# Kernel tuning notes

Hardware: AMD Instinct MI355X
Metric: run time of the kernel (lower is better)

The kernel has to match this reference:

```python
import jax, jax.numpy as jnp
import numpy as np

N_NODES = 100000


def _gcn_conv(x, W, b, src, dst, n_nodes):
    # PyG GCNConv: linear transform, add self-loops, symmetric deg normalization,
    # scatter-add aggregation at target nodes, then bias.
    h = x @ W  # [N, out]
    loops = jnp.arange(n_nodes, dtype=src.dtype)
    src2 = jnp.concatenate([src, loops])
    dst2 = jnp.concatenate([dst, loops])
    ones = jnp.ones(src2.shape[0], dtype=h.dtype)
    deg = jax.ops.segment_sum(ones, dst2, num_segments=n_nodes)  # in-degree incl. self-loop
    dinv = jnp.where(deg > 0, jax.lax.rsqrt(deg), 0.0)
    norm = dinv[src2] * dinv[dst2]  # [E+N]
    msg = h[src2] * norm[:, None]  # gather + weight, [E+N, out]
    out = jax.ops.segment_sum(msg, dst2, num_segments=n_nodes)
    return out + b


def setup_inputs() -> dict:
    key = jax.random.key(0)
    k1, k2, k3, k4 = jax.random.split(key, 4)
    n, e, f, h, c = N_NODES, 3200000, 512, 16, 32
    x = jax.random.normal(k1, (n, f), dtype=jnp.float32)
    edge_index = jax.random.randint(k2, (2, e), 0, n, dtype=jnp.int64)
    W1 = jax.random.normal(k3, (f, h), dtype=jnp.float32) * (1.0 / np.sqrt(f))
    b1 = jnp.zeros((h,), dtype=jnp.float32)
    W2 = jax.random.normal(k4, (h, c), dtype=jnp.float32) * (1.0 / np.sqrt(h))
    b2 = jnp.zeros((c,), dtype=jnp.float32)
    return {"x": x, "edge_index": edge_index, "W1": W1, "b1": b1, "W2": W2, "b2": b2}


def reference(x, edge_index, W1, b1, W2, b2):
    src, dst = edge_index[0], edge_index[1]
    n = x.shape[0]
    h = _gcn_conv(x, W1, b1, src, dst, n)
    h = jax.nn.relu(h)
    h = _gcn_conv(h, W2, b2, src, dst, n)
    return jax.nn.log_softmax(h, axis=1)
```

## Files before the change

kernel.cpp:

```cpp
#include <hip/hip_runtime.h>
#include <hip/hip_bf16.h>


#define BK 128
#define BKSH 7
#define MAXNB 1024
#define CHUNK 12800
#define SLAB 5120

typedef __attribute__((ext_vector_type(8))) short bf16x8;
typedef __attribute__((ext_vector_type(4))) float f32x4;

union ABpack { bf16x8 v; int i[4]; };

__device__ __forceinline__ int cvt2(float a, float b) {
    __hip_bfloat162 h = __float22bfloat162_rn(make_float2(a, b));
    return *reinterpret_cast<int*>(&h);
}
__device__ __forceinline__ unsigned short cvt1(float a) {
    __hip_bfloat16 h = __float2bfloat16(a);
    return *reinterpret_cast<unsigned short*>(&h);
}
__device__ __forceinline__ float b2f(unsigned short s) {
    return __uint_as_float(((unsigned)s) << 16);
}

__device__ __forceinline__ void load_lds16(const float* g, void* l) {
    __builtin_amdgcn_global_load_lds((const __attribute__((address_space(1))) void*)g,
                                     (__attribute__((address_space(3))) void*)l, 16, 0, 0);
}

__global__ __launch_bounds__(256) void k_init_cur(int* __restrict__ gcur, int NB) {
    int i = blockIdx.x * 256 + threadIdx.x;
    if (i < NB) gcur[i] = i * SLAB;
}

__global__ __launch_bounds__(256) void k_fill2(const int* __restrict__ src,
                                               const int* __restrict__ dst,
                                               int* __restrict__ gcur,
                                               int* __restrict__ gq, int E, int NB) {
    __shared__ int h[MAXNB];
    __shared__ int base[MAXNB];
    for (int t = threadIdx.x; t < NB; t += 256) h[t] = 0;
    __syncthreads();
    int e0 = blockIdx.x * CHUNK, e1 = min(E, e0 + CHUNK);
    for (int e = e0 + threadIdx.x; e < e1; e += 256)
        atomicAdd(&h[dst[e] >> BKSH], 1);
    __syncthreads();
    for (int t = threadIdx.x; t < NB; t += 256) {
        int c = h[t];
        base[t] = c ? atomicAdd(&gcur[t], c) : 0;
    }
    __syncthreads();
    for (int t = threadIdx.x; t < NB; t += 256) h[t] = 0;
    __syncthreads();
    for (int e = e0 + threadIdx.x; e < e1; e += 256) {
        int d = dst[e], b = d >> BKSH;
        int loc = atomicAdd(&h[b], 1);
        gq[base[b] + loc] = (src[e] << BKSH) | (d & (BK - 1));
    }
}

__global__ __launch_bounds__(256) void k_sortb(const int* __restrict__ gq,
                                               const int* __restrict__ gcur,
                                               int* __restrict__ gq2,
                                               int* __restrict__ offs,
                                               int* __restrict__ nend,
                                               float* __restrict__ dinv, int n) {
    __shared__ int cnt[BK];
    __shared__ int cur[BK];
    int b = blockIdx.x;
    int p0 = b * SLAB, p1 = gcur[b];
    if (threadIdx.x < BK) cnt[threadIdx.x] = 0;
    __syncthreads();
    for (int p = p0 + threadIdx.x; p < p1; p += 256)
        atomicAdd(&cnt[__builtin_nontemporal_load(gq + p) & (BK - 1)], 1);
    __syncthreads();
    if (threadIdx.x < BK) cur[threadIdx.x] = cnt[threadIdx.x];
    __syncthreads();
    for (int o = 1; o < BK; o <<= 1) {
        int v = (threadIdx.x < BK && threadIdx.x >= o) ? cur[threadIdx.x - o] : 0;
        __syncthreads();
        if (threadIdx.x < BK) cur[threadIdx.x] += v;
        __syncthreads();
    }
    if (threadIdx.x < BK) {
        int c = cnt[threadIdx.x];
        int excl = cur[threadIdx.x] - c;
        int node = (b << BKSH) + threadIdx.x;
        if (node < n) {
            offs[node] = p0 + excl;
            nend[node] = p0 + excl + c;
            dinv[node] = rsqrtf((float)(c + 1));
        }
        cur[threadIdx.x] = excl;
    }
    __syncthreads();
    for (int p = p0 + threadIdx.x; p < p1; p += 256) {
        int e = __builtin_nontemporal_load(gq + p);
        int loc = atomicAdd(&cur[e & (BK - 1)], 1);
        gq2[p0 + loc] = e >> BKSH;
    }
}

__global__ __launch_bounds__(256) void k_gemm_mfma(const float* __restrict__ x,
                                                   const float* __restrict__ W1,
                                                   const float* __restrict__ dinv,
                                                   unsigned short* __restrict__ gs1,
                                                   int n) {
    const int lane = threadIdx.x & 63;
    const int r = lane & 15;
    const int g4 = lane >> 4;
    const int wid = blockIdx.x * 4 + (threadIdx.x >> 6);
    const int nw = gridDim.x * 4;

    ABpack wf[16];
#pragma unroll
    for (int s = 0; s < 16; ++s) {
        int kb = s * 32 + g4 * 8;
#pragma unroll
        for (int j = 0; j < 4; ++j)
            wf[s].i[j] = cvt2(W1[(size_t)(kb + 2 * j) * 16 + r],
                              W1[(size_t)(kb + 2 * j + 1) * 16 + r]);
    }

    const int ntiles = (n + 15) >> 4;
    for (int tile = wid; tile < ntiles; tile += nw) {
        int m0 = tile << 4;
        int arow = m0 + r;
        if (arow >= n) arow = n - 1;
        const float* xp = x + (size_t)arow * 512 + g4 * 8;
        f32x4 acc = {0.f, 0.f, 0.f, 0.f};
#pragma unroll
        for (int s = 0; s < 16; ++s) {
            f32x4 f0 = __builtin_nontemporal_load(reinterpret_cast<const f32x4*>(xp + s * 32));
            f32x4 f1 = __builtin_nontemporal_load(reinterpret_cast<const f32x4*>(xp + s * 32 + 4));
            ABpack ah;
            ah.i[0] = cvt2(f0[0], f0[1]);
            ah.i[1] = cvt2(f0[2], f0[3]);
            ah.i[2] = cvt2(f1[0], f1[1]);
            ah.i[3] = cvt2(f1[2], f1[3]);
            acc = __builtin_amdgcn_mfma_f32_16x16x32_bf16(ah.v, wf[s].v, acc, 0, 0, 0);
        }
#pragma unroll
        for (int j = 0; j < 4; ++j) {
            int crow = m0 + g4 * 4 + j;
            if (crow < n) {
                float dvv = dinv[crow];
                gs1[(size_t)crow * 16 + r] = cvt1(acc[j] * dvv);
            }
        }
    }
}

__global__ __launch_bounds__(256) void k_agg_b(const unsigned short* __restrict__ featb,
                                               const int* __restrict__ gq2,
                                               const int* __restrict__ offs,
                                               const int* __restrict__ nend,
                                               const float* __restrict__ dinv,
                                               const float* __restrict__ bias,
                                               unsigned short* __restrict__ out_b,
                                               int n) {
    int t = blockIdx.x * 256 + threadIdx.x;
    int i = t >> 4, k = t & 15;
    if (i >= n) return;
    float acc = b2f(featb[(size_t)i * 16 + k]);
    int p = offs[i], p1 = nend[i];
    for (; p + 8 <= p1; p += 8) {
        int s0 = __builtin_nontemporal_load(gq2 + p);
        int s1 = __builtin_nontemporal_load(gq2 + p + 1);
        int s2 = __builtin_nontemporal_load(gq2 + p + 2);
        int s3 = __builtin_nontemporal_load(gq2 + p + 3);
        int s4 = __builtin_nontemporal_load(gq2 + p + 4);
        int s5 = __builtin_nontemporal_load(gq2 + p + 5);
        int s6 = __builtin_nontemporal_load(gq2 + p + 6);
        int s7 = __builtin_nontemporal_load(gq2 + p + 7);
        float v0 = b2f(featb[(size_t)s0 * 16 + k]);
        float v1 = b2f(featb[(size_t)s1 * 16 + k]);
        float v2 = b2f(featb[(size_t)s2 * 16 + k]);
        float v3 = b2f(featb[(size_t)s3 * 16 + k]);
        float v4 = b2f(featb[(size_t)s4 * 16 + k]);
        float v5 = b2f(featb[(size_t)s5 * 16 + k]);
        float v6 = b2f(featb[(size_t)s6 * 16 + k]);
        float v7 = b2f(featb[(size_t)s7 * 16 + k]);
        acc += ((v0 + v1) + (v2 + v3)) + ((v4 + v5) + (v6 + v7));
    }
    for (; p < p1; ++p)
        acc += b2f(featb[(size_t)__builtin_nontemporal_load(gq2 + p) * 16 + k]);
    float dvi = dinv[i];
    float v = fmaxf(dvi * acc + bias[k], 0.f) * dvi;
    out_b[(size_t)i * 16 + k] = cvt1(v);
}

__global__ __launch_bounds__(256) void k_agg_out(const unsigned short* __restrict__ featb,
                                                 const int* __restrict__ gq2,
                                                 const int* __restrict__ offs,
                                                 const int* __restrict__ nend,
                                                 const float* __restrict__ dinv,
                                                 const float* __restrict__ W2,
                                                 const float* __restrict__ b2,
                                                 float* __restrict__ out, int n) {
    __shared__ float Ws[16 * 33];
    __shared__ float bs[32];
    __shared__ float As[16][17];
    for (int t = threadIdx.x; t < 512; t += 256) Ws[(t >> 5) * 33 + (t & 31)] = W2[t];
    if (threadIdx.x < 32) bs[threadIdx.x] = b2[threadIdx.x];

    int t = blockIdx.x * 256 + threadIdx.x;
    int i = t >> 4, k = t & 15, nl = threadIdx.x >> 4;
    float acc = 0.f;
    if (i < n) {
        acc = b2f(featb[(size_t)i * 16 + k]);
        int p = offs[i], p1 = nend[i];
        for (; p + 8 <= p1; p += 8) {
            int s0 = __builtin_nontemporal_load(gq2 + p);
            int s1 = __builtin_nontemporal_load(gq2 + p + 1);
            int s2 = __builtin_nontemporal_load(gq2 + p + 2);
            int s3 = __builtin_nontemporal_load(gq2 + p + 3);
            int s4 = __builtin_nontemporal_load(gq2 + p + 4);
            int s5 = __builtin_nontemporal_load(gq2 + p + 5);
            int s6 = __builtin_nontemporal_load(gq2 + p + 6);
            int s7 = __builtin_nontemporal_load(gq2 + p + 7);
            float v0 = b2f(featb[(size_t)s0 * 16 + k]);
            float v1 = b2f(featb[(size_t)s1 * 16 + k]);
            float v2 = b2f(featb[(size_t)s2 * 16 + k]);
            float v3 = b2f(featb[(size_t)s3 * 16 + k]);
            float v4 = b2f(featb[(size_t)s4 * 16 + k]);
            float v5 = b2f(featb[(size_t)s5 * 16 + k]);
            float v6 = b2f(featb[(size_t)s6 * 16 + k]);
            float v7 = b2f(featb[(size_t)s7 * 16 + k]);
            acc += ((v0 + v1) + (v2 + v3)) + ((v4 + v5) + (v6 + v7));
        }
        for (; p < p1; ++p)
            acc += b2f(featb[(size_t)__builtin_nontemporal_load(gq2 + p) * 16 + k]);
        acc *= dinv[i];
    }
    As[nl][k] = acc;
    __syncthreads();
    if (i < n) {
        float v0 = bs[k], v1 = bs[k + 16];
#pragma unroll
        for (int kk = 0; kk < 16; ++kk) {
            float a = As[nl][kk];
            v0 += a * Ws[kk * 33 + k];
            v1 += a * Ws[kk * 33 + k + 16];
        }
        float m = fmaxf(v0, v1);
#pragma unroll
        for (int o = 8; o > 0; o >>= 1) m = fmaxf(m, __shfl_xor(m, o, 16));
        float pp = expf(v0 - m) + expf(v1 - m);
#pragma unroll
        for (int o = 8; o > 0; o >>= 1) pp += __shfl_xor(pp, o, 16);
        float lg = logf(pp);
        float* op = out + (size_t)i * 32;
        op[k] = v0 - m - lg;
        op[k + 16] = v1 - m - lg;
    }
}

__global__ __launch_bounds__(256) void k_zero_i(int* __restrict__ p, int n) {
    int i = blockIdx.x * 256 + threadIdx.x;
    if (i < n) p[i] = 0;
}

__global__ __launch_bounds__(256) void k_count(const int* __restrict__ dst,
                                               int* __restrict__ cnt, int E) {
    int e = blockIdx.x * 256 + threadIdx.x;
    if (e < E) atomicAdd(&cnt[dst[e]], 1);
}

__global__ __launch_bounds__(256) void k_dinv(const int* __restrict__ cnt,
                                              float* __restrict__ dinv, int n) {
    int i = blockIdx.x * 256 + threadIdx.x;
    if (i < n) dinv[i] = rsqrtf((float)(cnt[i] + 1));
}

__global__ __launch_bounds__(256) void k_gemm1(const float* __restrict__ x,
                                               const float* __restrict__ W1,
                                               const float* __restrict__ dinv,
                                               float* __restrict__ h1,
                                               float* __restrict__ r1self, int n) {
    __shared__ float Ws[8192];
    __shared__ float4 Xs[4][512];
    for (int t = threadIdx.x; t < 8192; t += 256) {
        int sa = t ^ (((t >> 9) & 1) << 4);
        Ws[sa] = W1[t];
    }
    __syncthreads();
    const int wave = threadIdx.x >> 6;
    const int lane = threadIdx.x & 63;
    const int q = lane & 15, g = lane >> 4;
    const int sr = lane >> 3, su = lane & 7;
    const int first = blockIdx.x * 4 + wave;
    const int stride = gridDim.x * 4;
    const int ngroups = (n + 7) >> 3;
    if (first >= ngroups) return;
    const int mygroups = (ngroups - first + stride - 1) / stride;
    const int T = mygroups * 4;
    char* xbase = (char*)(&Xs[wave][0]);
    auto stage = [&](int i) {
        int k = i >> 2, c = i & 3;
        int r0 = (first + k * stride) << 3;
        int row = r0 + sr;
        if (row >= n) row = n - 1;
        const float* gp = x + (size_t)row * 512 + c * 128 + su * 4;
        char* lb = xbase + (i & 1) * 4096;
#pragma unroll
        for (int m = 0; m < 4; ++m) load_lds16(gp + m * 32, lb + m * 1024);
    };
    stage(0);
    if (T > 1) stage(1);
    int issued = (T > 1) ? 2 : 1;
    float acc[8];
    const float4* xw = &Xs[wave][0];
    const int flip = (g & 1) << 4;
    for (int i = 0; i < T; ++i) {
        if (i < T - 1) asm volatile("s_waitcnt vmcnt(4)" ::: "memory");
        else           asm volatile("s_waitcnt vmcnt(0)" ::: "memory");
        int c = i & 3;
        const float4* xb = xw + (i & 1) * 256;
        if (c == 0) {
#pragma unroll
            for (int r = 0; r < 8; ++r) acc[r] = 0.f;
        }
        const int aW = 2048 * c + 512 * g + q;
#pragma unroll
        for (int t = 0; t < 8; ++t) {
            int tg = (t + g) & 7;
            float4 xv[8];
#pragma unroll
            for (int r = 0; r < 8; ++r) xv[r] = xb[g * 64 + r * 8 + tg];
            int a0 = aW + 64 * tg;
            float w0 = Ws[(a0) ^ flip];
            float w1 = Ws[(a0 + 16) ^ flip];
            float w2 = Ws[(a0 + 32) ^ flip];
            float w3 = Ws[(a0 + 48) ^ flip];
#pragma unroll
            for (int r = 0; r < 8; ++r)
                acc[r] += xv[r].x * w0 + xv[r].y * w1 + xv[r].z * w2 + xv[r].w * w3;
        }
        if (issued < T) { stage(issued); ++issued; }
        if (c == 3) {
            int r0 = (first + (i >> 2) * stride) << 3;
#pragma unroll
            for (int r = 0; r < 8; ++r) {
                acc[r] += __shfl_xor(acc[r], 16);
                acc[r] += __shfl_xor(acc[r], 32);
            }
            float v0 = 0.f, v1 = 0.f;
#pragma unroll
            for (int r = 0; r < 4; ++r)
                if (g == r) { v0 = acc[r]; v1 = acc[r + 4]; }
            int row0 = r0 + g, row1 = r0 + 4 + g;
            if (row0 < n) {
                h1[(size_t)row0 * 16 + q] = v0;
                if (r1self) { float dv = dinv[row0]; r1self[(size_t)row0 * 16 + q] = v0 * dv * dv; }
            }
            if (row1 < n) {
                h1[(size_t)row1 * 16 + q] = v1;
                if (r1self) { float dv = dinv[row1]; r1self[(size_t)row1 * 16 + q] = v1 * dv * dv; }
            }
        }
    }
}

__global__ __launch_bounds__(256) void k_scatter16(const int* __restrict__ src,
                                                   const int* __restrict__ dst,
                                                   const float* __restrict__ feat,
                                                   const float* __restrict__ dinv,
                                                   float* __restrict__ outf, int total) {
    int t = blockIdx.x * 256 + threadIdx.x;
    if (t >= total) return;
    int e = t >> 4, k = t & 15;
    int s = src[e], d = dst[e];
    float w = dinv[s] * dinv[d];
    unsafeAtomicAdd(&outf[(size_t)d * 16 + k], feat[(size_t)s * 16 + k] * w);
}

__global__ __launch_bounds__(256) void k_relu16(float* __restrict__ r1,
                                                const float* __restrict__ b1, int total) {
    int t = blockIdx.x * 256 + threadIdx.x;
    if (t < total) r1[t] = fmaxf(r1[t] + b1[t & 15], 0.f);
}

__global__ __launch_bounds__(256) void k_self16(const float* __restrict__ feat,
                                                const float* __restrict__ dinv,
                                                float* __restrict__ outf, int total) {
    int t = blockIdx.x * 256 + threadIdx.x;
    if (t >= total) return;
    float dv = dinv[t >> 4];
    outf[t] = feat[t] * dv * dv;
}

__global__ __launch_bounds__(256) void k_out(const float* __restrict__ a,
                                             const float* __restrict__ W2,
                                             const float* __restrict__ b2,
                                             float* __restrict__ out, int n) {
    __shared__ float Ws[16 * 33];
    __shared__ float bs[32];
    for (int t = threadIdx.x; t < 512; t += 256) Ws[(t >> 5) * 33 + (t & 31)] = W2[t];
    if (threadIdx.x < 32) bs[threadIdx.x] = b2[threadIdx.x];
    __syncthreads();
    int t = blockIdx.x * 256 + threadIdx.x;
    int i = t >> 5, c = t & 31;
    if (i >= n) return;
    const float4* ar = reinterpret_cast<const float4*>(a + (size_t)i * 16);
    float acc = bs[c];
#pragma unroll
    for (int kk = 0; kk < 4; ++kk) {
        float4 v = ar[kk];
        acc += v.x * Ws[(4 * kk + 0) * 33 + c];
        acc += v.y * Ws[(4 * kk + 1) * 33 + c];
        acc += v.z * Ws[(4 * kk + 2) * 33 + c];
        acc += v.w * Ws[(4 * kk + 3) * 33 + c];
    }
    float m = acc;
#pragma unroll
    for (int o = 16; o > 0; o >>= 1) m = fmaxf(m, __shfl_xor(m, o, 32));
    float p = expf(acc - m);
#pragma unroll
    for (int o = 16; o > 0; o >>= 1) p += __shfl_xor(p, o, 32);
    out[t] = acc - m - logf(p);
}

extern "C" void kernel_launch(void* const* d_in, const int* in_sizes, int n_in,
                              void* d_out, int out_size, void* d_ws, size_t ws_size,
                              hipStream_t stream) {
    const float* x  = (const float*)d_in[0];
    const int* ei   = (const int*)d_in[1];
    const float* W1 = (const float*)d_in[2];
    const float* b1 = (const float*)d_in[3];
    const float* W2 = (const float*)d_in[4];
    const float* b2 = (const float*)d_in[5];
    float* out = (float*)d_out;

    const int n = in_sizes[0] / 512;
    const int E = in_sizes[1] / 2;
    const int* src = ei;
    const int* dst = ei + E;
    const int NB = (n + BK - 1) >> BKSH;
    const int gfill = (E + CHUNK - 1) / CHUNK;
    const int ntiles = (n + 15) >> 4;
    const int ggemm = (ntiles + 3) / 4;

    float* ws = (float*)d_ws;

    size_t u_dinv  = 0;
    size_t u_foffs = u_dinv + n;
    size_t u_nend  = u_foffs + n;
    size_t u_gcur  = u_nend + n;
    size_t u_gq    = u_gcur + NB;
    size_t u_gq2   = u_gq + (size_t)NB * SLAB;
    size_t u_h1    = u_gq2 + (size_t)NB * SLAB;
    size_t u_r1    = u_h1 + 16 * (size_t)n;
    size_t need    = (u_r1 + 16 * (size_t)n) * 4;

    if (ws_size >= need && NB <= MAXNB) {
        float* dinv = ws + u_dinv;
        int* offs   = (int*)(ws + u_foffs);
        int* nend   = (int*)(ws + u_nend);
        int* gcur   = (int*)(ws + u_gcur);
        int* gq     = (int*)(ws + u_gq);
        int* gq2    = (int*)(ws + u_gq2);
        unsigned short* gs1b = (unsigned short*)(ws + u_h1);
        unsigned short* r1sb = (unsigned short*)(ws + u_r1);

        k_init_cur<<<(NB + 255) / 256, 256, 0, stream>>>(gcur, NB);
        k_fill2   <<<gfill, 256, 0, stream>>>(src, dst, gcur, gq, E, NB);
        k_sortb   <<<NB, 256, 0, stream>>>(gq, gcur, gq2, offs, nend, dinv, n);
        k_gemm_mfma<<<ggemm, 256, 0, stream>>>(x, W1, dinv, gs1b, n);
        k_agg_b   <<<(n * 16 + 255) / 256, 256, 0, stream>>>(gs1b, gq2, offs, nend,
                                                             dinv, b1, r1sb, n);
        k_agg_out <<<(n * 16 + 255) / 256, 256, 0, stream>>>(r1sb, gq2, offs, nend,
                                                             dinv, W2, b2, out, n);
    } else {
        float* dinv = ws;
        float* h1   = ws + n;
        float* r1   = ws + n + 16 * (size_t)n;
        int* cnt    = (int*)h1;
        float* agg2r = h1;

        const int total1 = E * 16;
        k_zero_i   <<<(n + 255) / 256, 256, 0, stream>>>(cnt, n);
        k_count    <<<(E + 255) / 256, 256, 0, stream>>>(dst, cnt, E);
        k_dinv     <<<(n + 255) / 256, 256, 0, stream>>>(cnt, dinv, n);
        k_gemm1    <<<1024, 256, 0, stream>>>(x, W1, dinv, h1, r1, n);
        k_scatter16<<<(total1 + 255) / 256, 256, 0, stream>>>(src, dst, h1, dinv, r1, total1);
        k_relu16   <<<(n * 16 + 255) / 256, 256, 0, stream>>>(r1, b1, n * 16);
        k_self16   <<<(n * 16 + 255) / 256, 256, 0, stream>>>(r1, dinv, agg2r, n * 16);
        k_scatter16<<<(total1 + 255) / 256, 256, 0, stream>>>(src, dst, r1, dinv, agg2r, total1);
        k_out      <<<(n * 32 + 255) / 256, 256, 0, stream>>>(agg2r, W2, b2, out, n);
    }
}
```

Before: 240.4 us.

## Stage X tiles through double-buffered swizzled LDS with split-K across waves in GEMM

The first-layer GEMM now streams each 16-row tile of x into a double-buffered LDS buffer with direct-to-LDS loads and an XOR swizzle. The four waves each take a quarter of K and combine partial sums through shared memory. The grid is fixed at 512 blocks with a prefetch of the next tile, meant to overlap HBM reads with compute and cut per-wave register use for W. The fill chunk size also shrinks, giving more fill blocks. In exchange it adds barriers, a reduction step and a separate tail path for row counts that are not a multiple of 16.

Result: slower. 249.2 us (+3.7%).

```diff
diff --git a/kernel.cpp b/kernel.cpp
--- a/kernel.cpp
+++ b/kernel.cpp
@@ -5,7 +5,7 @@
 #define BK 128
 #define BKSH 7
 #define MAXNB 1024
-#define CHUNK 12800
+#define CHUNK 3200
 #define SLAB 5120
 
 typedef __attribute__((ext_vector_type(8))) short bf16x8;
@@ -108,39 +108,107 @@
                                                    const float* __restrict__ dinv,
                                                    unsigned short* __restrict__ gs1,
                                                    int n) {
-    const int lane = threadIdx.x & 63;
+    __shared__ char Xs[2][32768];
+    __shared__ f32x4 red[256];
+    const int tid = threadIdx.x;
+    const int w = tid >> 6;
+    const int lane = tid & 63;
     const int r = lane & 15;
     const int g4 = lane >> 4;
-    const int wid = blockIdx.x * 4 + (threadIdx.x >> 6);
-    const int nw = gridDim.x * 4;
-
-    ABpack wf[16];
-#pragma unroll
-    for (int s = 0; s < 16; ++s) {
-        int kb = s * 32 + g4 * 8;
+
+    ABpack wf[4];
+#pragma unroll
+    for (int sl = 0; sl < 4; ++sl) {
+        int kb = (w * 4 + sl) * 32 + g4 * 8;
 #pragma unroll
         for (int j = 0; j < 4; ++j)
-            wf[s].i[j] = cvt2(W1[(size_t)(kb + 2 * j) * 16 + r],
-                              W1[(size_t)(kb + 2 * j + 1) * 16 + r]);
-    }
-
-    const int ntiles = (n + 15) >> 4;
-    for (int tile = wid; tile < ntiles; tile += nw) {
-        int m0 = tile << 4;
-        int arow = m0 + r;
-        if (arow >= n) arow = n - 1;
-        const float* xp = x + (size_t)arow * 512 + g4 * 8;
+            wf[sl].i[j] = cvt2(W1[(size_t)(kb + 2 * j) * 16 + r],
+                               W1[(size_t)(kb + 2 * j + 1) * 16 + r]);
+    }
+    asm volatile("s_waitcnt vmcnt(0)" ::: "memory");
+
+    auto stage = [&](int tile, int buf) {
+        const char* gp = (const char*)x + (size_t)tile * 32768;
+        char* lb = &Xs[buf][0];
+#pragma unroll
+        for (int c = 0; c < 8; ++c) {
+            int o = c * 4096 + tid * 16;
+            int g = o ^ (((o >> 11) & 7) << 4);
+            load_lds16((const float*)(gp + g), lb + o);
+        }
+    };
+
+    const int ntf = n >> 4;
+    int tile = blockIdx.x;
+    const int stride = gridDim.x;
+    if (tile < ntf) stage(tile, 0);
+    int buf = 0;
+    const int swz = (r & 7) << 4;
+
+    for (; tile < ntf; tile += stride) {
+        int nxt = tile + stride;
+        if (nxt < ntf) {
+            stage(nxt, buf ^ 1);
+            asm volatile("s_waitcnt vmcnt(8)" ::: "memory");
+        } else {
+            asm volatile("s_waitcnt vmcnt(0)" ::: "memory");
+        }
+        __builtin_amdgcn_s_barrier();
+        const char* lb = &Xs[buf][0];
         f32x4 acc = {0.f, 0.f, 0.f, 0.f};
 #pragma unroll
-        for (int s = 0; s < 16; ++s) {
-            f32x4 f0 = __builtin_nontemporal_load(reinterpret_cast<const f32x4*>(xp + s * 32));
-            f32x4 f1 = __builtin_nontemporal_load(reinterpret_cast<const f32x4*>(xp + s * 32 + 4));
+        for (int sl = 0; sl < 4; ++sl) {
+            int byte0 = r * 2048 + (w * 4 + sl) * 128 + g4 * 32;
+            f32x4 f0 = *reinterpret_cast<const f32x4*>(lb + (byte0 ^ swz));
+            f32x4 f1 = *reinterpret_cast<const f32x4*>(lb + ((byte0 + 16) ^ swz));
             ABpack ah;
             ah.i[0] = cvt2(f0[0], f0[1]);
             ah.i[1] = cvt2(f0[2], f0[3]);
             ah.i[2] = cvt2(f1[0], f1[1]);
             ah.i[3] = cvt2(f1[2], f1[3]);
-            acc = __builtin_amdgcn_mfma_f32_16x16x32_bf16(ah.v, wf[s].v, acc, 0, 0, 0);
+            acc = __builtin_amdgcn_mfma_f32_16x16x32_bf16(ah.v, wf[sl].v, acc, 0, 0, 0);
+        }
+        red[tid] = acc;
+        asm volatile("s_waitcnt lgkmcnt(0)" ::: "memory");
+        __builtin_amdgcn_s_barrier();
+        if (w == 0) {
+            f32x4 s0 = red[lane];
+            f32x4 s1 = red[64 + lane];
+            f32x4 s2 = red[128 + lane];
+            f32x4 s3 = red[192 + lane];
+            int m0 = tile << 4;
+#pragma unroll
+            for (int j = 0; j < 4; ++j) {
+                int crow = m0 + g4 * 4 + j;
+                float v = (s0[j] + s1[j]) + (s2[j] + s3[j]);
+                gs1[(size_t)crow * 16 + r] = cvt1(v * dinv[crow]);
+            }
+        }
+        buf ^= 1;
+    }
+
+    if ((n & 15) && blockIdx.x == 0 && w == 0) {
+        int m0 = ntf << 4;
+        int arow = m0 + r;
+        if (arow >= n) arow = n - 1;
+        const float* xp = x + (size_t)arow * 512 + g4 * 8;
+        f32x4 acc = {0.f, 0.f, 0.f, 0.f};
+#pragma unroll
+        for (int s = 0; s < 16; ++s) {
+            ABpack wfl;
+            int kb = s * 32 + g4 * 8;
+#pragma unroll
+            for (int j = 0; j < 4; ++j)
+                wfl.i[j] = cvt2(W1[(size_t)(kb + 2 * j) * 16 + r],
+                                W1[(size_t)(kb + 2 * j + 1) * 16 + r]);
+            f32x4 f0 = *reinterpret_cast<const f32x4*>(xp + s * 32);
+            f32x4 f1 = *reinterpret_cast<const f32x4*>(xp + s * 32 + 4);
+            ABpack ah;
+            ah.i[0] = cvt2(f0[0], f0[1]);
+            ah.i[1] = cvt2(f0[2], f0[3]);
+            ah.i[2] = cvt2(f1[0], f1[1]);
+            ah.i[3] = cvt2(f1[2], f1[3]);
+            acc = __builtin_amdgcn_mfma_f32_16x16x32_bf16(ah.v, wfl.v, acc, 0, 0, 0);
         }
 #pragma unroll
         for (int j = 0; j < 4; ++j) {
@@ -440,8 +508,6 @@
     const int* dst = ei + E;
     const int NB = (n + BK - 1) >> BKSH;
     const int gfill = (E + CHUNK - 1) / CHUNK;
-    const int ntiles = (n + 15) >> 4;
-    const int ggemm = (ntiles + 3) / 4;
 
     float* ws = (float*)d_ws;
 
@@ -468,7 +534,7 @@
         k_init_cur<<<(NB + 255) / 256, 256, 0, stream>>>(gcur, NB);
         k_fill2   <<<gfill, 256, 0, stream>>>(src, dst, gcur, gq, E, NB);
         k_sortb   <<<NB, 256, 0, stream>>>(gq, gcur, gq2, offs, nend, dinv, n);
-        k_gemm_mfma<<<ggemm, 256, 0, stream>>>(x, W1, dinv, gs1b, n);
+        k_gemm_mfma<<<512, 256, 0, stream>>>(x, W1, dinv, gs1b, n);
         k_agg_b   <<<(n * 16 + 255) / 256, 256, 0, stream>>>(gs1b, gq2, offs, nend,
                                                              dinv, b1, r1sb, n);
         k_agg_out <<<(n * 16 + 255) / 256, 256, 0, stream>>>(r1sb, gq2, offs, nend,
```
